# Kernel optimization log

Hardware: AMD Instinct MI355X
Metric: run time of the kernel (lower is better)

The kernel has to match this reference:

```python
import jax, jax.numpy as jnp
import numpy as np

BN = 1.0 / np.sqrt(1.0 + 1e-5)  # eval-mode BatchNorm at init (mean=0,var=1,gamma=1,beta=0)
EPS = 1e-5
WIN = 5
NH, HD = 8, 6

def _conv2d(x, w, ph, pw, groups=1):
    return jax.lax.conv_general_dilated(x, w, (1, 1), ((ph, ph), (pw, pw)),
        dimension_numbers=('NCHW', 'OIHW', 'NCHW'), feature_group_count=groups)

def _conv1d(x, w, p, groups=1):
    return jax.lax.conv_general_dilated(x, w, (1,), ((p, p),),
        dimension_numbers=('NCH', 'OIH', 'NCH'), feature_group_count=groups)

def _avgpool_t(x, k):
    s = jax.lax.reduce_window(x, 0.0, jax.lax.add, (1, 1, 1, k), (1, 1, 1, k), 'VALID')
    return s / k

def _ln(h, g, b):
    m = h.mean(-1, keepdims=True)
    v = h.var(-1, keepdims=True)  # biased, matches torch LayerNorm
    return (h - m) / jnp.sqrt(v + EPS) * g + b

def setup_inputs() -> dict:
    ks = jax.random.split(jax.random.key(0), 20)
    def n(i, shape, s=0.05):
        return jax.random.normal(ks[i], shape, dtype=jnp.float32) * s
    z = lambda *s: jnp.zeros(s, jnp.float32)
    o = lambda *s: jnp.ones(s, jnp.float32)
    return {
        'x': jax.random.normal(ks[0], (16, 1, 22, 16000), dtype=jnp.float32),
        'riem_w1': n(1, (253, 256)), 'riem_b1': z(256),
        'riem_w2': n(2, (256, 48)), 'riem_b2': z(48),
        'conv1_w': n(3, (16, 1, 1, 64)),
        'dw1_w': n(4, (32, 1, 22, 1)),
        'dw2_w': n(5, (32, 1, 1, 16)),
        'pw_w': n(6, (48, 32, 1, 1)),
        'tc1_w': n(7, (24, 2, 3)), 'tc1_b': z(24),
        'tc2_w': n(8, (48, 24, 1)), 'tc2_b': z(48),
        'fusion_proj': n(9, (48, 48), 0.15),
        'pos_enc': n(10, (1, 500, 48), 0.02),
        'ln1_g': o(4, 48), 'ln1_b': z(4, 48),
        'qkv_w': n(11, (4, 48, 144)), 'qkv_b': z(4, 144),
        'attn_proj_w': n(12, (4, 48, 48)), 'attn_proj_b': z(4, 48),
        'ln2_g': o(4, 48), 'ln2_b': z(4, 48),
        'ffn_w1': n(13, (4, 48, 192)), 'ffn_b1': z(4, 192),
        'ffn_w2': n(14, (4, 192, 48)), 'ffn_b2': z(4, 48),
        'cls_ln_g': o(48), 'cls_ln_b': z(48),
        'cls_w': n(15, (48, 4), 0.1), 'cls_b': z(4),
    }

def _forward(x, riem_w1, riem_b1, riem_w2, riem_b2, conv1_w, dw1_w, dw2_w, pw_w,
             tc1_w, tc1_b, tc2_w, tc2_b, fusion_proj, pos_enc,
             ln1_g, ln1_b, qkv_w, qkv_b, attn_proj_w, attn_proj_b,
             ln2_g, ln2_b, ffn_w1, ffn_b1, ffn_w2, ffn_b2,
             cls_ln_g, cls_ln_b, cls_w, cls_b):
    B = x.shape[0]
    # ---- Riemannian geometry branch ----
    xr = x[:, 0]                                   # (B, 22, T)
    C, T = xr.shape[1], xr.shape[2]
    xc = xr - xr.mean(-1, keepdims=True)
    cov = jnp.einsum('bct,bdt->bcd', xc, xc) / (T - 1)
    I = jnp.eye(C, dtype=x.dtype)
    cov = cov + I * 1e-5
    tr = jnp.trace(cov, axis1=1, axis2=2)
    cov = cov + I * (tr.mean() * 1e-3)
    L = jnp.linalg.cholesky(cov)
    dL = jnp.diagonal(L, axis1=-2, axis2=-1)
    log_cov = L * jnp.log(jnp.clip(dL, 1e-10))[:, None, :]   # L @ diag(log(diag L))
    iu = jnp.triu_indices(C)
    flat = log_cov[:, iu[0], iu[1]]                # (B, 253)
    r_feat = (jax.nn.elu(flat @ riem_w1 + riem_b1) @ riem_w2 + riem_b2)[:, None, :]
    # ---- Lightweight CNN branch (BatchNorms in eval = constant scale) ----
    h = _conv2d(x, conv1_w, 0, 32) * BN
    h = jax.nn.elu(_conv2d(h, dw1_w, 0, 0, groups=16) * BN)
    h = _avgpool_t(h, 8)
    h = _conv2d(h, dw2_w, 0, 8, groups=32) * BN
    h = jax.nn.elu(_conv2d(h, pw_w, 0, 0) * BN)
    h = _avgpool_t(h, 8)                            # (B, 48, 1, L)
    feat = jnp.transpose(h[:, :, 0, :], (0, 2, 1))  # (B, L, 48)
    t = _conv1d(jnp.transpose(feat, (0, 2, 1)), tc1_w, 1, groups=24) + tc1_b[None, :, None]
    t = jax.nn.gelu(t * BN, approximate=False)
    t = _conv1d(t, tc2_w, 0) + tc2_b[None, :, None]
    feat = feat + jnp.transpose(t, (0, 2, 1))
    # ---- Fusion + positional encoding ----
    fused = jnp.concatenate([r_feat, feat], axis=1) @ fusion_proj
    N = fused.shape[1]
    fused = fused + pos_enc[:, :N]
    # ---- Sparse (banded) transformer blocks ----
    idx = jnp.arange(N)
    band = jnp.abs(idx[:, None] - idx[None, :]) <= WIN   # allowed positions
    scale = HD ** -0.5
    for i in range(4):
        res = fused
        hh = _ln(fused, ln1_g[i], ln1_b[i])
        qkv = (hh @ qkv_w[i] + qkv_b[i]).reshape(B, N, 3, NH, HD)
        q = jnp.transpose(qkv[:, :, 0], (0, 2, 1, 3))
        k = jnp.transpose(qkv[:, :, 1], (0, 2, 1, 3))
        v = jnp.transpose(qkv[:, :, 2], (0, 2, 1, 3))
        att = jnp.einsum('bhqd,bhkd->bhqk', q, k) * scale
        att = jax.nn.softmax(jnp.where(band, att, -jnp.inf), axis=-1)
        o = jnp.einsum('bhqk,bhkd->bhqd', att, v)
        o = jnp.transpose(o, (0, 2, 1, 3)).reshape(B, N, NH * HD)
        fused = res + (o @ attn_proj_w[i] + attn_proj_b[i])
        res = fused
        hh = _ln(fused, ln2_g[i], ln2_b[i])
        hh = jax.nn.gelu(hh @ ffn_w1[i] + ffn_b1[i], approximate=False) @ ffn_w2[i] + ffn_b2[i]
        fused = res + hh
    g = fused.mean(axis=1)
    g = _ln(g, cls_ln_g, cls_ln_b)
    return g @ cls_w + cls_b

def reference(x, riem_w1, riem_b1, riem_w2, riem_b2, conv1_w, dw1_w, dw2_w, pw_w,
              tc1_w, tc1_b, tc2_w, tc2_b, fusion_proj, pos_enc,
              ln1_g, ln1_b, qkv_w, qkv_b, attn_proj_w, attn_proj_b,
              ln2_g, ln2_b, ffn_w1, ffn_b1, ffn_w2, ffn_b2,
              cls_ln_g, cls_ln_b, cls_w, cls_b):
    return _forward(x, riem_w1, riem_b1, riem_w2, riem_b2, conv1_w, dw1_w, dw2_w, pw_w,
                    tc1_w, tc1_b, tc2_w, tc2_b, fusion_proj, pos_enc,
                    ln1_g, ln1_b, qkv_w, qkv_b, attn_proj_w, attn_proj_b,
                    ln2_g, ln2_b, ffn_w1, ffn_b1, ffn_w2, ffn_b2,
                    cls_ln_g, cls_ln_b, cls_w, cls_b)
```

## Files before the change

kernel.cpp:

```cpp
#include <hip/hip_runtime.h>
#include <hip/hip_bf16.h>
#include <math.h>

#define BN_C 0.9999950000375f
#define NB 16
#define NC 22
#define NT 16000
#define NPAIR 253
#define NSEQ 251
#define ND 48
#define TR 8
#define TE 18

__device__ __forceinline__ unsigned short f2bf(float f) {
    union { float f; unsigned int u; } v; v.f = f;
    unsigned int r = v.u + 0x7fff + ((v.u >> 16) & 1);
    return (unsigned short)(r >> 16);
}
__device__ __forceinline__ float bf2f(unsigned short s) {
    union { unsigned int u; float f; } v; v.u = ((unsigned int)s) << 16;
    return v.f;
}

__global__ __launch_bounds__(256) void k_y(const float* __restrict__ x,
                                           const float* __restrict__ dw1,
                                           __hip_bfloat16* __restrict__ y) {
    int gid = blockIdx.x * 256 + threadIdx.x;
    int b = gid / 8000, tp = gid % 8000;
    int t = tp * 2;
    const float* xb = x + (size_t)b * NC * NT + t;
    float a0[32], a1[32];
    #pragma unroll
    for (int j = 0; j < 32; j++) { a0[j] = 0.f; a1[j] = 0.f; }
    for (int h = 0; h < NC; h++) {
        float2 xv = *(const float2*)&xb[(size_t)h * NT];
        #pragma unroll
        for (int j = 0; j < 32; j++) {
            float w = dw1[j * NC + h];
            a0[j] += w * xv.x; a1[j] += w * xv.y;
        }
    }
    unsigned int* yo = (unsigned int*)(y + (size_t)b * 32 * NT + t);
    #pragma unroll
    for (int j = 0; j < 32; j++) {
        unsigned int pk = (unsigned int)f2bf(a0[j]) | ((unsigned int)f2bf(a1[j]) << 16);
        yo[j * (NT / 2)] = pk;
    }
}

#define TCHUNK 500
#define XROW 504
__global__ __launch_bounds__(256) void k_covS(const float* __restrict__ x,
                                              float* __restrict__ covS,
                                              float* __restrict__ sums) {
    int chunk = blockIdx.x, b = blockIdx.y;
    int t0 = chunk * TCHUNK;
    __shared__ unsigned short xs[NC * XROW];
    const float* xp = x + (size_t)b * NC * NT + t0;
    for (int i = threadIdx.x; i < NC * 126; i += 256) {
        int c = i / 126, q = i % 126;
        unsigned long long pk = 0ull;
        if (q < 125) {
            float4 v = *(const float4*)&xp[(size_t)c * NT + 4 * q];
            pk = (unsigned long long)f2bf(v.x) | ((unsigned long long)f2bf(v.y) << 16)
               | ((unsigned long long)f2bf(v.z) << 32) | ((unsigned long long)f2bf(v.w) << 48);
        }
        *(unsigned long long*)&xs[c * XROW + 4 * q] = pk;
    }
    __syncthreads();
    int p = threadIdx.x;
    if (p < NPAIR) {
        int c = 0, r = p;
        while (r >= NC - c) { r -= NC - c; c++; }
        int d = c + r;
        const unsigned short* xc = &xs[c * XROW];
        const unsigned short* xd = &xs[d * XROW];
        float a0 = 0, a1 = 0, a2 = 0, a3 = 0;
        float s0 = 0, s1 = 0, s2 = 0, s3 = 0;
        for (int t = 0; t < XROW; t += 8) {
            uint4 pc = *(const uint4*)&xc[t];
            uint4 pd = *(const uint4*)&xd[t];
            float c0 = bf2f((unsigned short)pc.x), c1 = bf2f((unsigned short)(pc.x >> 16));
            float c2 = bf2f((unsigned short)pc.y), c3 = bf2f((unsigned short)(pc.y >> 16));
            float c4 = bf2f((unsigned short)pc.z), c5 = bf2f((unsigned short)(pc.z >> 16));
            float c6 = bf2f((unsigned short)pc.w), c7 = bf2f((unsigned short)(pc.w >> 16));
            float d0 = bf2f((unsigned short)pd.x), d1 = bf2f((unsigned short)(pd.x >> 16));
            float d2 = bf2f((unsigned short)pd.y), d3 = bf2f((unsigned short)(pd.y >> 16));
            float d4 = bf2f((unsigned short)pd.z), d5 = bf2f((unsigned short)(pd.z >> 16));
            float d6 = bf2f((unsigned short)pd.w), d7 = bf2f((unsigned short)(pd.w >> 16));
            a0 += c0 * d0 + c4 * d4; a1 += c1 * d1 + c5 * d5;
            a2 += c2 * d2 + c6 * d6; a3 += c3 * d3 + c7 * d7;
            s0 += c0 + c4; s1 += c1 + c5; s2 += c2 + c6; s3 += c3 + c7;
        }
        atomicAdd(&covS[b * NPAIR + p], (a0 + a1) + (a2 + a3));
        if (c == d) atomicAdd(&sums[b * NC + c], (s0 + s1) + (s2 + s3));
    }
}

__global__ __launch_bounds__(256) void k_cholfeat(
    const float* __restrict__ covS, const float* __restrict__ sums,
    const float* __restrict__ w1, const float* __restrict__ b1,
    const float* __restrict__ w2, const float* __restrict__ b2,
    float* __restrict__ rfeat) {
    int b = blockIdx.x, t = threadIdx.x;
    __shared__ float covL[484];
    __shared__ float trS[NB];
    __shared__ float dvs[NC];
    __shared__ float hid[256];
    __shared__ float part[4][ND];
    if (t < NB) trS[t] = 0.f;
    __syncthreads();
    if (t < NPAIR) {
        int c = 0, r = t;
        while (r >= NC - c) { r -= NC - c; c++; }
        int d = c + r;
        float v = (covS[b * NPAIR + t] - sums[b * NC + c] * sums[b * NC + d] / (float)NT)
                  / (float)(NT - 1);
        if (c == d) v += 1e-5f;
        covL[c * NC + d] = v;
        covL[d * NC + c] = v;
    }
    for (int i = t; i < NB * NC; i += 256) {
        int bb = i / NC, c = i % NC;
        int pos = c * NC - c * (c - 1) / 2;
        float sc = sums[bb * NC + c];
        float v = (covS[bb * NPAIR + pos] - sc * sc / (float)NT) / (float)(NT - 1) + 1e-5f;
        atomicAdd(&trS[bb], v);
    }
    __syncthreads();
    float trs = 0.f;
    for (int i = 0; i < NB; i++) trs += trS[i];
    float trm = trs * (0.001f / (float)NB);
    if (t < 64) {
        int lane = t;
        float a[NC];
        #pragma unroll
        for (int j = 0; j < NC; j++) {
            float v = (lane < NC) ? covL[lane * NC + j] : 0.f;
            a[j] = v + ((j == lane) ? trm : 0.f);
        }
        float diagv = 1.f;
        #pragma unroll
        for (int k = 0; k < NC; k++) {
            float akk = __shfl(a[k], k);
            float dk = sqrtf(akk);
            if (lane == k) { a[k] = dk; diagv = dk; }
            else if (lane > k) a[k] /= dk;
            float myak = a[k];
            #pragma unroll
            for (int j = k + 1; j < NC; j++) {
                float ljk = __shfl(myak, j);
                if (lane >= j) a[j] -= myak * ljk;
            }
        }
        if (lane < NC) dvs[lane] = diagv * logf(fmaxf(diagv, 1e-10f));
    }
    __syncthreads();
    {
        float acc = b1[t];
        #pragma unroll
        for (int d = 0; d < NC; d++) {
            int pos = d * NC - d * (d - 1) / 2;
            acc += dvs[d] * w1[pos * 256 + t];
        }
        hid[t] = (acc > 0.f) ? acc : expm1f(acc);
    }
    __syncthreads();
    if (t < 192) {
        int col = t % ND, kc = t / ND;
        float a = 0.f;
        #pragma unroll
        for (int i = 0; i < 64; i++) a += hid[kc * 64 + i] * w2[(kc * 64 + i) * ND + col];
        part[kc][col] = a;
    }
    __syncthreads();
    if (t < ND)
        rfeat[b * ND + t] = b2[t] + part[0][t] + part[1][t] + part[2][t] + part[3][t];
}

#define CT2 512
__global__ __launch_bounds__(256) void k_conv64(const __hip_bfloat16* __restrict__ y,
                                                const float* __restrict__ c1w,
                                                float* __restrict__ p) {
    int tile = blockIdx.x, j = blockIdx.y, b = blockIdx.z;
    int u0 = tile * CT2;
    __shared__ float yt[4680];
    const __hip_bfloat16* yp = y + ((size_t)(b * 32 + j)) * NT;
    int tbase = u0 * 8 - 32;
    for (int q = threadIdx.x; q < 2080; q += 256) {
        int i = 2 * q;
        int tq = tbase + i;
        float v0 = 0.f, v1 = 0.f;
        if (tq >= 0 && tq + 1 < NT) {
            unsigned int pk = *(const unsigned int*)(yp + tq);
            v0 = bf2f((unsigned short)pk); v1 = bf2f((unsigned short)(pk >> 16));
        } else {
            if (tq >= 0 && tq < NT) v0 = __bfloat162float(yp[tq]);
            if (tq + 1 >= 0 && tq + 1 < NT) v1 = __bfloat162float(yp[tq + 1]);
        }
        yt[i + (i >> 3)] = v0;
        int i1 = i + 1;
        yt[i1 + (i1 >> 3)] = v1;
    }
    __syncthreads();
    const float* cf = c1w + (j >> 1) * 64;
    int u = u0 + 2 * threadIdx.x;
    if (u < 2000) {
        int off = 16 * threadIdx.x;
        float acc[16];
        #pragma unroll
        for (int s = 0; s < 16; s++) acc[s] = 0.f;
        #pragma unroll
        for (int kb = 0; kb < 64; kb += 16) {
            float Y[31];
            #pragma unroll
            for (int m = 0; m < 31; m++) {
                int idx = off + kb + m;
                Y[m] = yt[idx + (idx >> 3)];
            }
            #pragma unroll
            for (int k = 0; k < 16; k++) {
                float c = cf[kb + k];
                #pragma unroll
                for (int s = 0; s < 16; s++) acc[s] += c * Y[k + s];
            }
        }
        const float bn2 = BN_C * BN_C;
        float pv0 = 0.f, pv1 = 0.f;
        #pragma unroll
        for (int s = 0; s < 8; s++) {
            float z0 = bn2 * acc[s];
            pv0 += (z0 > 0.f) ? z0 : expm1f(z0);
            float z1 = bn2 * acc[8 + s];
            pv1 += (z1 > 0.f) ? z1 : expm1f(z1);
        }
        size_t base = ((size_t)(b * 32 + j)) * 2000;
        p[base + u] = pv0 * 0.125f;
        if (u + 1 < 2000) p[base + u + 1] = pv1 * 0.125f;
    }
}

__global__ __launch_bounds__(256) void k_stage2fuse(
    const float* __restrict__ p, const float* __restrict__ dw2,
    const float* __restrict__ pw, const float* __restrict__ rfeat,
    const float* __restrict__ tc1w, const float* __restrict__ tc1b,
    const float* __restrict__ tc2w, const float* __restrict__ tc2b,
    const float* __restrict__ fp, const float* __restrict__ pe,
    float* __restrict__ fused) {
    int bx = blockIdx.x, b = blockIdx.y, t = threadIdx.x;
    __shared__ float pt[32][64];
    __shared__ float dval[32][48];
    __shared__ float feat6[6][ND];
    __shared__ float w2s[512];
    __shared__ float pws[1536];
    __shared__ float g1[4][24];
    __shared__ float row[4][ND];
    for (int i = t; i < 512; i += 256) w2s[i] = dw2[i];
    for (int i = t; i < 1536; i += 256) pws[i] = pw[i];
    int gt0 = 32 * bx - 24;
    for (int i = t; i < 32 * 63; i += 256) {
        int j = i / 63, tt = i % 63;
        int gt = gt0 + tt;
        pt[j][tt] = (gt >= 0 && gt < 2000) ? p[((size_t)(b * 32 + j)) * 2000 + gt] : 0.f;
    }
    __syncthreads();
    for (int i = t; i < 1536; i += 256) {
        int j = i / 48, su = i % 48;
        int w = su >> 3, s = su & 7;
        float a = 0.f;
        #pragma unroll
        for (int k = 0; k < 16; k++) a += w2s[j * 16 + k] * pt[j][8 * w + s + k];
        dval[j][su] = a * BN_C;
    }
    __syncthreads();
    for (int i = t; i < 6 * ND; i += 256) {
        int w = i / ND, col = i % ND;
        int u2 = 4 * bx - 2 + w;
        float acc = 0.f;
        if (u2 >= 0 && u2 < 250) {
            float wreg[32];
            #pragma unroll
            for (int j = 0; j < 32; j++) wreg[j] = pws[col * 32 + j];
            #pragma unroll
            for (int s = 0; s < 8; s++) {
                float e = 0.f;
                #pragma unroll
                for (int j = 0; j < 32; j++) e += wreg[j] * dval[j][w * 8 + s];
                e *= BN_C;
                acc += (e > 0.f) ? e : expm1f(e);
            }
            acc *= 0.125f;
        }
        feat6[w][col] = acc;
    }
    __syncthreads();
    if (t < 96) {
        int sub = t / 24, m = t % 24;
        int n = 4 * bx + sub;
        if (n >= 1 && n < NSEQ) {
            float a = tc1b[m];
            #pragma unroll
            for (int k = 0; k < 3; k++) {
                int w = sub + k;
                a += tc1w[m * 6 + k] * feat6[w][2 * m]
                   + tc1w[m * 6 + 3 + k] * feat6[w][2 * m + 1];
            }
            float z = a * BN_C;
            g1[sub][m] = 0.5f * z * (1.f + erff(z * 0.70710678f));
        }
    }
    __syncthreads();
    if (t < 192) {
        int sub = t / ND, col = t % ND;
        int n = 4 * bx + sub;
        if (n < NSEQ) {
            if (n == 0) {
                row[sub][col] = rfeat[b * ND + col];
            } else {
                float a = tc2b[col];
                #pragma unroll
                for (int m = 0; m < 24; m++) a += tc2w[col * 24 + m] * g1[sub][m];
                row[sub][col] = feat6[sub + 1][col] + a;
            }
        }
    }
    __syncthreads();
    if (t < 192) {
        int sub = t / ND, col = t % ND;
        int n = 4 * bx + sub;
        if (n < NSEQ) {
            float o = pe[n * ND + col];
            for (int c = 0; c < ND; c++) o += row[sub][c] * fp[c * ND + col];
            fused[((size_t)b * NSEQ + n) * ND + col] = o;
        }
    }
}

__global__ __launch_bounds__(512) void k_layer(
    float* __restrict__ fused,
    const float* __restrict__ g1v, const float* __restrict__ b1v,
    const float* __restrict__ qw, const float* __restrict__ qb,
    const float* __restrict__ apw, const float* __restrict__ apb,
    const float* __restrict__ g2v, const float* __restrict__ b2v,
    const float* __restrict__ w1, const float* __restrict__ fb1,
    const float* __restrict__ w2, const float* __restrict__ fb2) {
    int tile = blockIdx.x, b = blockIdx.y;
    int n0 = tile * TR;
    int t = threadIdx.x;
    __shared__ float row[TE][ND];
    __shared__ float hh[TE][ND];
    __shared__ float qkvS[TE * 144];
    __shared__ float ob[TR][ND];
    __shared__ float nrow[TR][ND];
    __shared__ float mrs[TE][2];
    __shared__ float part[4][TR][ND];
    float* hid = qkvS;

    for (int i = t; i < TE * ND; i += 512) {
        int e = i / ND, c = i % ND;
        int n = n0 - 5 + e;
        row[e][c] = (n >= 0 && n < NSEQ) ? fused[((size_t)b * NSEQ + n) * ND + c] : 0.f;
    }
    __syncthreads();
    if (t < TE * 16) {
        int r = t >> 4, i = t & 15;
        float v0 = row[r][i], v1 = row[r][i + 16], v2 = row[r][i + 32];
        float s = v0 + v1 + v2;
        s += __shfl_down(s, 8, 16); s += __shfl_down(s, 4, 16);
        s += __shfl_down(s, 2, 16); s += __shfl_down(s, 1, 16);
        float m = __shfl(s, 0, 16) * (1.f / ND);
        float d0 = v0 - m, d1 = v1 - m, d2 = v2 - m;
        float q = d0 * d0 + d1 * d1 + d2 * d2;
        q += __shfl_down(q, 8, 16); q += __shfl_down(q, 4, 16);
        q += __shfl_down(q, 2, 16); q += __shfl_down(q, 1, 16);
        if (i == 0) { mrs[r][0] = m; mrs[r][1] = rsqrtf(q * (1.f / ND) + 1e-5f); }
    }
    __syncthreads();
    for (int i = t; i < TE * ND; i += 512) {
        int e = i / ND, c = i % ND;
        hh[e][c] = (row[e][c] - mrs[e][0]) * mrs[e][1] * g1v[c] + b1v[c];
    }
    __syncthreads();
    if (t < 288) {
        int col = t % 144, eg = t / 144;
        float w[ND];
        #pragma unroll
        for (int c = 0; c < ND; c++) w[c] = qw[c * 144 + col];
        float bias = qb[col];
        for (int e = eg * 9; e < eg * 9 + 9; e++) {
            float a = bias;
            #pragma unroll
            for (int c = 0; c < ND; c++) a += hh[e][c] * w[c];
            qkvS[e * 144 + col] = a;
        }
    }
    __syncthreads();
    if (t < TR * 8) {
        int r = t >> 3, h = t & 7;
        int n = n0 + r;
        if (n < NSEQ) {
            int k0 = n - 5; if (k0 < 0) k0 = 0;
            int k1 = n + 5; if (k1 > NSEQ - 1) k1 = NSEQ - 1;
            int nk = k1 - k0 + 1;
            float q[6];
            #pragma unroll
            for (int d = 0; d < 6; d++) q[d] = qkvS[(r + 5) * 144 + h * 6 + d];
            float sc[11];
            float mx = -1e30f;
            for (int ki = 0; ki < nk; ki++) {
                int e = k0 + ki - n0 + 5;
                float s = 0;
                #pragma unroll
                for (int d = 0; d < 6; d++) s += q[d] * qkvS[e * 144 + 48 + h * 6 + d];
                s *= 0.4082482904638631f;
                sc[ki] = s; mx = fmaxf(mx, s);
            }
            float sum = 0;
            for (int ki = 0; ki < nk; ki++) { float e = expf(sc[ki] - mx); sc[ki] = e; sum += e; }
            float inv = 1.f / sum;
            float o[6] = {0, 0, 0, 0, 0, 0};
            for (int ki = 0; ki < nk; ki++) {
                int e = k0 + ki - n0 + 5;
                float pv = sc[ki] * inv;
                #pragma unroll
                for (int d = 0; d < 6; d++) o[d] += pv * qkvS[e * 144 + 96 + h * 6 + d];
            }
            #pragma unroll
            for (int d = 0; d < 6; d++) ob[r][h * 6 + d] = o[d];
        } else {
            #pragma unroll
            for (int d = 0; d < 6; d++) ob[r][h * 6 + d] = 0.f;
        }
    }
    __syncthreads();
    if (t < TR * ND) {
        int r = t / ND, col = t % ND;
        float a = apb[col];
        #pragma unroll
        for (int c = 0; c < ND; c++) a += ob[r][c] * apw[c * ND + col];
        nrow[r][col] = row[r + 5][col] + a;
    }
    __syncthreads();
    if (t < TR * 16) {
        int r = t >> 4, i = t & 15;
        float v0 = nrow[r][i], v1 = nrow[r][i + 16], v2 = nrow[r][i + 32];
        float s = v0 + v1 + v2;
        s += __shfl_down(s, 8, 16); s += __shfl_down(s, 4, 16);
        s += __shfl_down(s, 2, 16); s += __shfl_down(s, 1, 16);
        float m = __shfl(s, 0, 16) * (1.f / ND);
        float d0 = v0 - m, d1 = v1 - m, d2 = v2 - m;
        float q = d0 * d0 + d1 * d1 + d2 * d2;
        q += __shfl_down(q, 8, 16); q += __shfl_down(q, 4, 16);
        q += __shfl_down(q, 2, 16); q += __shfl_down(q, 1, 16);
        if (i == 0) { mrs[r][0] = m; mrs[r][1] = rsqrtf(q * (1.f / ND) + 1e-5f); }
    }
    __syncthreads();
    if (t < TR * ND) {
        int r = t / ND, c = t % ND;
        hh[r][c] = (nrow[r][c] - mrs[r][0]) * mrs[r][1] * g2v[c] + b2v[c];
    }
    __syncthreads();
    if (t < 384) {
        int col = t % 192, rg = t / 192;
        float w[ND];
        #pragma unroll
        for (int c = 0; c < ND; c++) w[c] = w1[c * 192 + col];
        float bias = fb1[col];
        for (int r = rg * 4; r < rg * 4 + 4; r++) {
            float a = bias;
            #pragma unroll
            for (int c = 0; c < ND; c++) a += hh[r][c] * w[c];
            hid[r * 192 + col] = 0.5f * a * (1.f + erff(a * 0.70710678f));
        }
    }
    __syncthreads();
    if (t < 384) {
        int col = t % ND, kc = (t / ND) & 3, rh = t / 192;
        float w[ND];
        #pragma unroll
        for (int i2 = 0; i2 < ND; i2++) w[i2] = w2[(kc * ND + i2) * ND + col];
        for (int r = rh * 4; r < rh * 4 + 4; r++) {
            float a = 0;
            #pragma unroll
            for (int i2 = 0; i2 < ND; i2++) a += hid[r * 192 + kc * ND + i2] * w[i2];
            part[kc][r][col] = a;
        }
    }
    __syncthreads();
    for (int i = t; i < TR * ND; i += 512) {
        int r = i / ND, c = i % ND;
        int n = n0 + r;
        if (n < NSEQ) {
            fused[((size_t)b * NSEQ + n) * ND + c] =
                nrow[r][c] + fb2[c] + part[0][r][c] + part[1][r][c] + part[2][r][c] + part[3][r][c];
        }
    }
}

__global__ void k_head(const float* __restrict__ fused, const float* __restrict__ lg,
                       const float* __restrict__ lb, const float* __restrict__ cw,
                       const float* __restrict__ cb, float* __restrict__ out) {
    int b = blockIdx.x, t = threadIdx.x;
    __shared__ float part[4][ND];
    __shared__ float gg[ND], mv[2];
    if (t < 192) {
        int col = t % ND, qt = t / ND;
        int nA = qt * 63;
        int nB = (nA + 63 < NSEQ) ? nA + 63 : NSEQ;
        float s = 0.f;
        for (int n = nA; n < nB; n++) s += fused[((size_t)b * NSEQ + n) * ND + col];
        part[qt][col] = s;
    }
    __syncthreads();
    if (t < ND) gg[t] = (part[0][t] + part[1][t] + part[2][t] + part[3][t]) * (1.f / NSEQ);
    __syncthreads();
    if (t == 0) {
        float m = 0;
        for (int c = 0; c < ND; c++) m += gg[c];
        m /= (float)ND;
        float v = 0;
        for (int c = 0; c < ND; c++) { float dd = gg[c] - m; v += dd * dd; }
        v /= (float)ND;
        mv[0] = m; mv[1] = rsqrtf(v + 1e-5f);
    }
    __syncthreads();
    if (t < ND) gg[t] = (gg[t] - mv[0]) * mv[1] * lg[t] + lb[t];
    __syncthreads();
    if (t < 4) {
        float a = cb[t];
        for (int c = 0; c < ND; c++) a += gg[c] * cw[c * 4 + t];
        out[b * 4 + t] = a;
    }
}

extern "C" void kernel_launch(void* const* d_in, const int* in_sizes, int n_in,
                              void* d_out, int out_size, void* d_ws, size_t ws_size,
                              hipStream_t stream) {
    const float* x       = (const float*)d_in[0];
    const float* riem_w1 = (const float*)d_in[1];
    const float* riem_b1 = (const float*)d_in[2];
    const float* riem_w2 = (const float*)d_in[3];
    const float* riem_b2 = (const float*)d_in[4];
    const float* conv1_w = (const float*)d_in[5];
    const float* dw1_w   = (const float*)d_in[6];
    const float* dw2_w   = (const float*)d_in[7];
    const float* pw_w    = (const float*)d_in[8];
    const float* tc1_w   = (const float*)d_in[9];
    const float* tc1_b   = (const float*)d_in[10];
    const float* tc2_w   = (const float*)d_in[11];
    const float* tc2_b   = (const float*)d_in[12];
    const float* fusion  = (const float*)d_in[13];
    const float* pos_enc = (const float*)d_in[14];
    const float* ln1_g   = (const float*)d_in[15];
    const float* ln1_b   = (const float*)d_in[16];
    const float* qkv_w   = (const float*)d_in[17];
    const float* qkv_b   = (const float*)d_in[18];
    const float* apw     = (const float*)d_in[19];
    const float* apb     = (const float*)d_in[20];
    const float* ln2_g   = (const float*)d_in[21];
    const float* ln2_b   = (const float*)d_in[22];
    const float* ffn_w1  = (const float*)d_in[23];
    const float* ffn_b1  = (const float*)d_in[24];
    const float* ffn_w2  = (const float*)d_in[25];
    const float* ffn_b2  = (const float*)d_in[26];
    const float* cls_g   = (const float*)d_in[27];
    const float* cls_b_  = (const float*)d_in[28];
    const float* cls_w   = (const float*)d_in[29];
    const float* cls_bb  = (const float*)d_in[30];
    float* out = (float*)d_out;

    float* ws = (float*)d_ws;
    float* covS  = ws;
    float* sums  = ws + 4048;
    float* rfeat = ws + 4400;
    float* fused = ws + 5168;
    float* pbuf  = ws + 197936;
    __hip_bfloat16* ybuf = (__hip_bfloat16*)(ws + 1221936);

    hipMemsetAsync(covS, 0, 4400 * sizeof(float), stream);

    k_y<<<500, 256, 0, stream>>>(x, dw1_w, ybuf);
    k_covS<<<dim3(32, NB), 256, 0, stream>>>(x, covS, sums);
    k_cholfeat<<<NB, 256, 0, stream>>>(covS, sums, riem_w1, riem_b1, riem_w2, riem_b2, rfeat);

    k_conv64<<<dim3(4, 32, NB), 256, 0, stream>>>(ybuf, conv1_w, pbuf);
    k_stage2fuse<<<dim3(63, NB), 256, 0, stream>>>(pbuf, dw2_w, pw_w, rfeat,
                                                   tc1_w, tc1_b, tc2_w, tc2_b,
                                                   fusion, pos_enc, fused);

    for (int i = 0; i < 4; i++) {
        k_layer<<<dim3(32, NB), 512, 0, stream>>>(
            fused, ln1_g + i * 48, ln1_b + i * 48, qkv_w + i * 6912, qkv_b + i * 144,
            apw + i * 2304, apb + i * 48, ln2_g + i * 48, ln2_b + i * 48,
            ffn_w1 + i * 9216, ffn_b1 + i * 192, ffn_w2 + i * 9216, ffn_b2 + i * 48);
    }

    k_head<<<NB, 256, 0, stream>>>(fused, cls_g, cls_b_, cls_w, cls_bb, out);
}
```

Measured before the change: 298.6 us.

## Merge independent stage kernels into combined launches and use fast exp

Merges the k_y and k_covS kernels into one launch whose blocks branch by index, and merges the conv64 and Cholesky-feature kernels the same way, cutting two launches and letting independent work run concurrently. The conv kernel now gives each thread one output instead of two, using smaller tiles and more blocks, which lowers register pressure. expm1f/expf are replaced with __expf-based ELU and softmax, trading a little accuracy near zero for cheaper transcendentals. The merged kernels share one shared-memory footprint sized for the larger branch, which may reduce occupancy for the smaller one.

```diff
diff --git a/kernel.cpp b/kernel.cpp
--- a/kernel.cpp
+++ b/kernel.cpp
@@ -21,222 +21,218 @@
     union { unsigned int u; float f; } v; v.u = ((unsigned int)s) << 16;
     return v.f;
 }
-
-__global__ __launch_bounds__(256) void k_y(const float* __restrict__ x,
-                                           const float* __restrict__ dw1,
-                                           __hip_bfloat16* __restrict__ y) {
-    int gid = blockIdx.x * 256 + threadIdx.x;
-    int b = gid / 8000, tp = gid % 8000;
-    int t = tp * 2;
-    const float* xb = x + (size_t)b * NC * NT + t;
-    float a0[32], a1[32];
-    #pragma unroll
-    for (int j = 0; j < 32; j++) { a0[j] = 0.f; a1[j] = 0.f; }
-    for (int h = 0; h < NC; h++) {
-        float2 xv = *(const float2*)&xb[(size_t)h * NT];
-        #pragma unroll
-        for (int j = 0; j < 32; j++) {
-            float w = dw1[j * NC + h];
-            a0[j] += w * xv.x; a1[j] += w * xv.y;
-        }
-    }
-    unsigned int* yo = (unsigned int*)(y + (size_t)b * 32 * NT + t);
-    #pragma unroll
-    for (int j = 0; j < 32; j++) {
-        unsigned int pk = (unsigned int)f2bf(a0[j]) | ((unsigned int)f2bf(a1[j]) << 16);
-        yo[j * (NT / 2)] = pk;
-    }
+__device__ __forceinline__ float elu_fast(float z) {
+    return (z > 0.f) ? z : (__expf(z) - 1.f);
 }
 
 #define TCHUNK 500
 #define XROW 504
-__global__ __launch_bounds__(256) void k_covS(const float* __restrict__ x,
+__global__ __launch_bounds__(256) void k_ycov(const float* __restrict__ x,
+                                              const float* __restrict__ dw1,
+                                              __hip_bfloat16* __restrict__ y,
                                               float* __restrict__ covS,
                                               float* __restrict__ sums) {
-    int chunk = blockIdx.x, b = blockIdx.y;
-    int t0 = chunk * TCHUNK;
     __shared__ unsigned short xs[NC * XROW];
-    const float* xp = x + (size_t)b * NC * NT + t0;
-    for (int i = threadIdx.x; i < NC * 126; i += 256) {
-        int c = i / 126, q = i % 126;
-        unsigned long long pk = 0ull;
-        if (q < 125) {
-            float4 v = *(const float4*)&xp[(size_t)c * NT + 4 * q];
-            pk = (unsigned long long)f2bf(v.x) | ((unsigned long long)f2bf(v.y) << 16)
-               | ((unsigned long long)f2bf(v.z) << 32) | ((unsigned long long)f2bf(v.w) << 48);
-        }
-        *(unsigned long long*)&xs[c * XROW + 4 * q] = pk;
-    }
-    __syncthreads();
-    int p = threadIdx.x;
-    if (p < NPAIR) {
-        int c = 0, r = p;
-        while (r >= NC - c) { r -= NC - c; c++; }
-        int d = c + r;
-        const unsigned short* xc = &xs[c * XROW];
-        const unsigned short* xd = &xs[d * XROW];
-        float a0 = 0, a1 = 0, a2 = 0, a3 = 0;
-        float s0 = 0, s1 = 0, s2 = 0, s3 = 0;
-        for (int t = 0; t < XROW; t += 8) {
-            uint4 pc = *(const uint4*)&xc[t];
-            uint4 pd = *(const uint4*)&xd[t];
-            float c0 = bf2f((unsigned short)pc.x), c1 = bf2f((unsigned short)(pc.x >> 16));
-            float c2 = bf2f((unsigned short)pc.y), c3 = bf2f((unsigned short)(pc.y >> 16));
-            float c4 = bf2f((unsigned short)pc.z), c5 = bf2f((unsigned short)(pc.z >> 16));
-            float c6 = bf2f((unsigned short)pc.w), c7 = bf2f((unsigned short)(pc.w >> 16));
-            float d0 = bf2f((unsigned short)pd.x), d1 = bf2f((unsigned short)(pd.x >> 16));
-            float d2 = bf2f((unsigned short)pd.y), d3 = bf2f((unsigned short)(pd.y >> 16));
-            float d4 = bf2f((unsigned short)pd.z), d5 = bf2f((unsigned short)(pd.z >> 16));
-            float d6 = bf2f((unsigned short)pd.w), d7 = bf2f((unsigned short)(pd.w >> 16));
-            a0 += c0 * d0 + c4 * d4; a1 += c1 * d1 + c5 * d5;
-            a2 += c2 * d2 + c6 * d6; a3 += c3 * d3 + c7 * d7;
-            s0 += c0 + c4; s1 += c1 + c5; s2 += c2 + c6; s3 += c3 + c7;
-        }
-        atomicAdd(&covS[b * NPAIR + p], (a0 + a1) + (a2 + a3));
-        if (c == d) atomicAdd(&sums[b * NC + c], (s0 + s1) + (s2 + s3));
-    }
-}
-
-__global__ __launch_bounds__(256) void k_cholfeat(
+    if (blockIdx.x < 512) {
+        int chunk = blockIdx.x & 31, b = blockIdx.x >> 5;
+        int t0 = chunk * TCHUNK;
+        const float* xp = x + (size_t)b * NC * NT + t0;
+        for (int i = threadIdx.x; i < NC * 126; i += 256) {
+            int c = i / 126, q = i % 126;
+            unsigned long long pk = 0ull;
+            if (q < 125) {
+                float4 v = *(const float4*)&xp[(size_t)c * NT + 4 * q];
+                pk = (unsigned long long)f2bf(v.x) | ((unsigned long long)f2bf(v.y) << 16)
+                   | ((unsigned long long)f2bf(v.z) << 32) | ((unsigned long long)f2bf(v.w) << 48);
+            }
+            *(unsigned long long*)&xs[c * XROW + 4 * q] = pk;
+        }
+        __syncthreads();
+        int p = threadIdx.x;
+        if (p < NPAIR) {
+            int c = 0, r = p;
+            while (r >= NC - c) { r -= NC - c; c++; }
+            int d = c + r;
+            const unsigned short* xc = &xs[c * XROW];
+            const unsigned short* xd = &xs[d * XROW];
+            float a0 = 0, a1 = 0, a2 = 0, a3 = 0;
+            float s0 = 0, s1 = 0, s2 = 0, s3 = 0;
+            for (int t = 0; t < XROW; t += 8) {
+                uint4 pc = *(const uint4*)&xc[t];
+                uint4 pd = *(const uint4*)&xd[t];
+                float c0 = bf2f((unsigned short)pc.x), c1 = bf2f((unsigned short)(pc.x >> 16));
+                float c2 = bf2f((unsigned short)pc.y), c3 = bf2f((unsigned short)(pc.y >> 16));
+                float c4 = bf2f((unsigned short)pc.z), c5 = bf2f((unsigned short)(pc.z >> 16));
+                float c6 = bf2f((unsigned short)pc.w), c7 = bf2f((unsigned short)(pc.w >> 16));
+                float d0 = bf2f((unsigned short)pd.x), d1 = bf2f((unsigned short)(pd.x >> 16));
+                float d2 = bf2f((unsigned short)pd.y), d3 = bf2f((unsigned short)(pd.y >> 16));
+                float d4 = bf2f((unsigned short)pd.z), d5 = bf2f((unsigned short)(pd.z >> 16));
+                float d6 = bf2f((unsigned short)pd.w), d7 = bf2f((unsigned short)(pd.w >> 16));
+                a0 += c0 * d0 + c4 * d4; a1 += c1 * d1 + c5 * d5;
+                a2 += c2 * d2 + c6 * d6; a3 += c3 * d3 + c7 * d7;
+                s0 += c0 + c4; s1 += c1 + c5; s2 += c2 + c6; s3 += c3 + c7;
+            }
+            atomicAdd(&covS[b * NPAIR + p], (a0 + a1) + (a2 + a3));
+            if (c == d) atomicAdd(&sums[b * NC + c], (s0 + s1) + (s2 + s3));
+        }
+    } else {
+        int gid = (blockIdx.x - 512) * 256 + threadIdx.x;
+        int b = gid / 8000, tp = gid % 8000;
+        int t = tp * 2;
+        const float* xb = x + (size_t)b * NC * NT + t;
+        float a0[32], a1[32];
+        #pragma unroll
+        for (int j = 0; j < 32; j++) { a0[j] = 0.f; a1[j] = 0.f; }
+        for (int h = 0; h < NC; h++) {
+            float2 xv = *(const float2*)&xb[(size_t)h * NT];
+            #pragma unroll
+            for (int j = 0; j < 32; j++) {
+                float w = dw1[j * NC + h];
+                a0[j] += w * xv.x; a1[j] += w * xv.y;
+            }
+        }
+        unsigned int* yo = (unsigned int*)(y + (size_t)b * 32 * NT + t);
+        #pragma unroll
+        for (int j = 0; j < 32; j++) {
+            unsigned int pk = (unsigned int)f2bf(a0[j]) | ((unsigned int)f2bf(a1[j]) << 16);
+            yo[j * (NT / 2)] = pk;
+        }
+    }
+}
+
+__global__ __launch_bounds__(256) void k_convchol(
+    const __hip_bfloat16* __restrict__ y, const float* __restrict__ c1w,
+    float* __restrict__ p,
     const float* __restrict__ covS, const float* __restrict__ sums,
     const float* __restrict__ w1, const float* __restrict__ b1,
     const float* __restrict__ w2, const float* __restrict__ b2,
     float* __restrict__ rfeat) {
-    int b = blockIdx.x, t = threadIdx.x;
+    __shared__ float yt[2376];
     __shared__ float covL[484];
     __shared__ float trS[NB];
     __shared__ float dvs[NC];
     __shared__ float hid[256];
     __shared__ float part[4][ND];
-    if (t < NB) trS[t] = 0.f;
-    __syncthreads();
-    if (t < NPAIR) {
-        int c = 0, r = t;
-        while (r >= NC - c) { r -= NC - c; c++; }
-        int d = c + r;
-        float v = (covS[b * NPAIR + t] - sums[b * NC + c] * sums[b * NC + d] / (float)NT)
-                  / (float)(NT - 1);
-        if (c == d) v += 1e-5f;
-        covL[c * NC + d] = v;
-        covL[d * NC + c] = v;
-    }
-    for (int i = t; i < NB * NC; i += 256) {
-        int bb = i / NC, c = i % NC;
-        int pos = c * NC - c * (c - 1) / 2;
-        float sc = sums[bb * NC + c];
-        float v = (covS[bb * NPAIR + pos] - sc * sc / (float)NT) / (float)(NT - 1) + 1e-5f;
-        atomicAdd(&trS[bb], v);
-    }
-    __syncthreads();
-    float trs = 0.f;
-    for (int i = 0; i < NB; i++) trs += trS[i];
-    float trm = trs * (0.001f / (float)NB);
-    if (t < 64) {
-        int lane = t;
-        float a[NC];
-        #pragma unroll
-        for (int j = 0; j < NC; j++) {
-            float v = (lane < NC) ? covL[lane * NC + j] : 0.f;
-            a[j] = v + ((j == lane) ? trm : 0.f);
-        }
-        float diagv = 1.f;
-        #pragma unroll
-        for (int k = 0; k < NC; k++) {
-            float akk = __shfl(a[k], k);
-            float dk = sqrtf(akk);
-            if (lane == k) { a[k] = dk; diagv = dk; }
-            else if (lane > k) a[k] /= dk;
-            float myak = a[k];
-            #pragma unroll
-            for (int j = k + 1; j < NC; j++) {
-                float ljk = __shfl(myak, j);
-                if (lane >= j) a[j] -= myak * ljk;
-            }
-        }
-        if (lane < NC) dvs[lane] = diagv * logf(fmaxf(diagv, 1e-10f));
-    }
-    __syncthreads();
-    {
-        float acc = b1[t];
-        #pragma unroll
-        for (int d = 0; d < NC; d++) {
-            int pos = d * NC - d * (d - 1) / 2;
-            acc += dvs[d] * w1[pos * 256 + t];
-        }
-        hid[t] = (acc > 0.f) ? acc : expm1f(acc);
-    }
-    __syncthreads();
-    if (t < 192) {
-        int col = t % ND, kc = t / ND;
-        float a = 0.f;
-        #pragma unroll
-        for (int i = 0; i < 64; i++) a += hid[kc * 64 + i] * w2[(kc * 64 + i) * ND + col];
-        part[kc][col] = a;
-    }
-    __syncthreads();
-    if (t < ND)
-        rfeat[b * ND + t] = b2[t] + part[0][t] + part[1][t] + part[2][t] + part[3][t];
-}
-
-#define CT2 512
-__global__ __launch_bounds__(256) void k_conv64(const __hip_bfloat16* __restrict__ y,
-                                                const float* __restrict__ c1w,
-                                                float* __restrict__ p) {
-    int tile = blockIdx.x, j = blockIdx.y, b = blockIdx.z;
-    int u0 = tile * CT2;
-    __shared__ float yt[4680];
-    const __hip_bfloat16* yp = y + ((size_t)(b * 32 + j)) * NT;
-    int tbase = u0 * 8 - 32;
-    for (int q = threadIdx.x; q < 2080; q += 256) {
-        int i = 2 * q;
-        int tq = tbase + i;
-        float v0 = 0.f, v1 = 0.f;
-        if (tq >= 0 && tq + 1 < NT) {
-            unsigned int pk = *(const unsigned int*)(yp + tq);
-            v0 = bf2f((unsigned short)pk); v1 = bf2f((unsigned short)(pk >> 16));
-        } else {
-            if (tq >= 0 && tq < NT) v0 = __bfloat162float(yp[tq]);
-            if (tq + 1 >= 0 && tq + 1 < NT) v1 = __bfloat162float(yp[tq + 1]);
-        }
-        yt[i + (i >> 3)] = v0;
-        int i1 = i + 1;
-        yt[i1 + (i1 >> 3)] = v1;
-    }
-    __syncthreads();
-    const float* cf = c1w + (j >> 1) * 64;
-    int u = u0 + 2 * threadIdx.x;
-    if (u < 2000) {
-        int off = 16 * threadIdx.x;
-        float acc[16];
-        #pragma unroll
-        for (int s = 0; s < 16; s++) acc[s] = 0.f;
-        #pragma unroll
-        for (int kb = 0; kb < 64; kb += 16) {
-            float Y[31];
-            #pragma unroll
-            for (int m = 0; m < 31; m++) {
-                int idx = off + kb + m;
-                Y[m] = yt[idx + (idx >> 3)];
-            }
-            #pragma unroll
-            for (int k = 0; k < 16; k++) {
-                float c = cf[kb + k];
-                #pragma unroll
-                for (int s = 0; s < 16; s++) acc[s] += c * Y[k + s];
-            }
-        }
-        const float bn2 = BN_C * BN_C;
-        float pv0 = 0.f, pv1 = 0.f;
-        #pragma unroll
-        for (int s = 0; s < 8; s++) {
-            float z0 = bn2 * acc[s];
-            pv0 += (z0 > 0.f) ? z0 : expm1f(z0);
-            float z1 = bn2 * acc[8 + s];
-            pv1 += (z1 > 0.f) ? z1 : expm1f(z1);
-        }
-        size_t base = ((size_t)(b * 32 + j)) * 2000;
-        p[base + u] = pv0 * 0.125f;
-        if (u + 1 < 2000) p[base + u + 1] = pv1 * 0.125f;
+    if (blockIdx.x >= NB) {
+        int bx = blockIdx.x - NB;
+        int tile = bx & 7, j = (bx >> 3) & 31, b = bx >> 8;
+        int u0 = tile * 256;
+        const __hip_bfloat16* yp = y + ((size_t)(b * 32 + j)) * NT;
+        int tbase = u0 * 8 - 32;
+        for (int q = threadIdx.x; q < 1056; q += 256) {
+            int i = 2 * q;
+            int tq = tbase + i;
+            float v0 = 0.f, v1 = 0.f;
+            if (tq >= 0 && tq + 1 < NT) {
+                unsigned int pk = *(const unsigned int*)(yp + tq);
+                v0 = bf2f((unsigned short)pk); v1 = bf2f((unsigned short)(pk >> 16));
+            } else {
+                if (tq >= 0 && tq < NT) v0 = __bfloat162float(yp[tq]);
+                if (tq + 1 >= 0 && tq + 1 < NT) v1 = __bfloat162float(yp[tq + 1]);
+            }
+            yt[i + (i >> 3)] = v0;
+            int i1 = i + 1;
+            yt[i1 + (i1 >> 3)] = v1;
+        }
+        __syncthreads();
+        const float* cf = c1w + (j >> 1) * 64;
+        int u = u0 + threadIdx.x;
+        if (u < 2000) {
+            int off = 8 * threadIdx.x;
+            float acc[8];
+            #pragma unroll
+            for (int s = 0; s < 8; s++) acc[s] = 0.f;
+            #pragma unroll
+            for (int kb = 0; kb < 64; kb += 16) {
+                float Yb[23];
+                #pragma unroll
+                for (int m = 0; m < 23; m++) {
+                    int idx = off + kb + m;
+                    Yb[m] = yt[idx + (idx >> 3)];
+                }
+                #pragma unroll
+                for (int k = 0; k < 16; k++) {
+                    float c = cf[kb + k];
+                    #pragma unroll
+                    for (int s = 0; s < 8; s++) acc[s] += c * Yb[k + s];
+                }
+            }
+            const float bn2 = BN_C * BN_C;
+            float pv = 0.f;
+            #pragma unroll
+            for (int s = 0; s < 8; s++) pv += elu_fast(bn2 * acc[s]);
+            p[((size_t)(b * 32 + j)) * 2000 + u] = pv * 0.125f;
+        }
+    } else {
+        int b = blockIdx.x, t = threadIdx.x;
+        if (t < NB) trS[t] = 0.f;
+        __syncthreads();
+        if (t < NPAIR) {
+            int c = 0, r = t;
+            while (r >= NC - c) { r -= NC - c; c++; }
+            int d = c + r;
+            float v = (covS[b * NPAIR + t] - sums[b * NC + c] * sums[b * NC + d] / (float)NT)
+                      / (float)(NT - 1);
+            if (c == d) v += 1e-5f;
+            covL[c * NC + d] = v;
+            covL[d * NC + c] = v;
+        }
+        for (int i = t; i < NB * NC; i += 256) {
+            int bb = i / NC, c = i % NC;
+            int pos = c * NC - c * (c - 1) / 2;
+            float sc = sums[bb * NC + c];
+            float v = (covS[bb * NPAIR + pos] - sc * sc / (float)NT) / (float)(NT - 1) + 1e-5f;
+            atomicAdd(&trS[bb], v);
+        }
+        __syncthreads();
+        float trs = 0.f;
+        for (int i = 0; i < NB; i++) trs += trS[i];
+        float trm = trs * (0.001f / (float)NB);
+        if (t < 64) {
+            int lane = t;
+            float a[NC];
+            #pragma unroll
+            for (int j = 0; j < NC; j++) {
+                float v = (lane < NC) ? covL[lane * NC + j] : 0.f;
+                a[j] = v + ((j == lane) ? trm : 0.f);
+            }
+            float diagv = 1.f;
+            #pragma unroll
+            for (int k = 0; k < NC; k++) {
+                float akk = __shfl(a[k], k);
+                float dk = sqrtf(akk);
+                if (lane == k) { a[k] = dk; diagv = dk; }
+                else if (lane > k) a[k] /= dk;
+                float myak = a[k];
+                #pragma unroll
+                for (int j = k + 1; j < NC; j++) {
+                    float ljk = __shfl(myak, j);
+                    if (lane >= j) a[j] -= myak * ljk;
+                }
+            }
+            if (lane < NC) dvs[lane] = diagv * logf(fmaxf(diagv, 1e-10f));
+        }
+        __syncthreads();
+        {
+            float acc = b1[t];
+            #pragma unroll
+            for (int d = 0; d < NC; d++) {
+                int pos = d * NC - d * (d - 1) / 2;
+                acc += dvs[d] * w1[pos * 256 + t];
+            }
+            hid[t] = elu_fast(acc);
+        }
+        __syncthreads();
+        if (t < 192) {
+            int col = t % ND, kc = t / ND;
+            float a = 0.f;
+            #pragma unroll
+            for (int i = 0; i < 64; i++) a += hid[kc * 64 + i] * w2[(kc * 64 + i) * ND + col];
+            part[kc][col] = a;
+        }
+        __syncthreads();
+        if (t < ND)
+            rfeat[b * ND + t] = b2[t] + part[0][t] + part[1][t] + part[2][t] + part[3][t];
     }
 }
 
@@ -286,8 +282,7 @@
                 float e = 0.f;
                 #pragma unroll
                 for (int j = 0; j < 32; j++) e += wreg[j] * dval[j][w * 8 + s];
-                e *= BN_C;
-                acc += (e > 0.f) ? e : expm1f(e);
+                acc += elu_fast(e * BN_C);
             }
             acc *= 0.125f;
         }
@@ -416,7 +411,7 @@
                 sc[ki] = s; mx = fmaxf(mx, s);
             }
             float sum = 0;
-            for (int ki = 0; ki < nk; ki++) { float e = expf(sc[ki] - mx); sc[ki] = e; sum += e; }
+            for (int ki = 0; ki < nk; ki++) { float e = __expf(sc[ki] - mx); sc[ki] = e; sum += e; }
             float inv = 1.f / sum;
             float o[6] = {0, 0, 0, 0, 0, 0};
             for (int ki = 0; ki < nk; ki++) {
@@ -579,11 +574,9 @@
 
     hipMemsetAsync(covS, 0, 4400 * sizeof(float), stream);
 
-    k_y<<<500, 256, 0, stream>>>(x, dw1_w, ybuf);
-    k_covS<<<dim3(32, NB), 256, 0, stream>>>(x, covS, sums);
-    k_cholfeat<<<NB, 256, 0, stream>>>(covS, sums, riem_w1, riem_b1, riem_w2, riem_b2, rfeat);
-
-    k_conv64<<<dim3(4, 32, NB), 256, 0, stream>>>(ybuf, conv1_w, pbuf);
+    k_ycov<<<1012, 256, 0, stream>>>(x, dw1_w, ybuf, covS, sums);
+    k_convchol<<<4112, 256, 0, stream>>>(ybuf, conv1_w, pbuf, covS, sums,
+                                         riem_w1, riem_b1, riem_w2, riem_b2, rfeat);
     k_stage2fuse<<<dim3(63, NB), 256, 0, stream>>>(pbuf, dw2_w, pw_w, rfeat,
                                                    tc1_w, tc1_b, tc2_w, tc2_b,
                                                    fusion, pos_enc, fused);
```

Result: faster. 274.1 us (-8.2%).
